# Kernel tuning notes

Measured on AMD Instinct MI355X. Metric: run time of the kernel, lower is better.

The kernel has to match this reference:

```python
import jax, jax.numpy as jnp
import numpy as np

# Paired binary-tree layout over 20 inputs: widths 20->10->5->3->2->1.
# Odd trailing element is carried through unchanged. Node counts per layer
# sum to 19 nodes per tree; 19 trees total.
LAYER_WIDTHS = [20, 10, 5, 3, 2]  # widths at the input of each pairing layer
NODE_COUNTS = [10, 5, 2, 1, 1]    # pairs formed at each layer (sum = 19)
EPS = 1e-6


def setup_inputs() -> dict:
    key = jax.random.key(0)
    k1, k2, k3, k4 = jax.random.split(key, 4)
    B = 1_000_000
    p1 = jax.random.randint(k1, (B,), 0, 10)
    p2 = jax.random.randint(k2, (B,), 0, 10)
    c20 = jax.random.uniform(k3, (B, 20), dtype=jnp.float32)  # fuzzy truth values in [0,1]
    # raw andness params: one per node (19) per tree (19)
    w_raw = jax.random.normal(k4, (19, 19), dtype=jnp.float32)
    return {"p1": p1, "p2": p2, "c20": c20, "w_raw": w_raw}


def _multi_tree_forward(c20, w_raw):
    B = c20.shape[0]
    T = 19  # number of trees
    # andness in (0,1): convex mix between AND (min) and OR (max)
    w = jax.nn.sigmoid(w_raw)  # [T, 19]
    # all 19 trees see the same 20D input -> vectorize trees as a dim
    x = jnp.broadcast_to(c20[:, None, :], (B, T, 20))  # [B, T, 20]
    off = 0
    for width, n in zip(LAYER_WIDTHS, NODE_COUNTS):
        a = x[:, :, 0:2 * n:2]   # left children  [B, T, n]
        b = x[:, :, 1:2 * n:2]   # right children [B, T, n]
        wn = w[:, off:off + n][None, :, :]  # [1, T, n]
        y = wn * jnp.minimum(a, b) + (1.0 - wn) * jnp.maximum(a, b)
        if width % 2 == 1:  # carry the unpaired trailing element through
            y = jnp.concatenate([y, x[:, :, -1:]], axis=-1)
        x = y
        off += n
    out = x[:, :, 0]  # [B, 19] root of each tree
    return jnp.clip(out, EPS, 1.0 - EPS)


def reference(p1, p2, c20, w_raw):
    # p1/p2 are part of the original signature but unused by the forward math
    return _multi_tree_forward(c20, w_raw)
```

## Files before the change

kernel.cpp:

```cpp
#include <hip/hip_runtime.h>

#define EPS_F 1e-6f

__global__ void sigmoid_w_kernel(const float* __restrict__ w_raw,
                                 float* __restrict__ w) {
    int i = threadIdx.x;
    if (i < 361) {
        w[i] = 1.0f / (1.0f + expf(-w_raw[i]));
    }
}

__device__ __forceinline__ float mixf(float a, float b, float wv) {
    float mn = fminf(a, b);
    float mx = fmaxf(a, b);
    return fmaf(wv, mn - mx, mx);
}

__global__ __launch_bounds__(256) void tree_forward_kernel(
    const float* __restrict__ c20,
    const float* __restrict__ w,
    float* __restrict__ out,
    int B)
{
    int s = blockIdx.x * blockDim.x + threadIdx.x;
    if (s >= B) return;

    float x[20];
    const float4* src = reinterpret_cast<const float4*>(c20 + (size_t)s * 20);
    #pragma unroll
    for (int q = 0; q < 5; ++q) {
        float4 v = src[q];
        x[4*q + 0] = v.x;
        x[4*q + 1] = v.y;
        x[4*q + 2] = v.z;
        x[4*q + 3] = v.w;
    }

    float* dst = out + (size_t)s * 19;

    #pragma unroll
    for (int t = 0; t < 19; ++t) {
        const float* wr = w + t * 19;

        float y[10];
        #pragma unroll
        for (int k = 0; k < 10; ++k)
            y[k] = mixf(x[2*k], x[2*k + 1], wr[k]);

        float z[5];
        #pragma unroll
        for (int k = 0; k < 5; ++k)
            z[k] = mixf(y[2*k], y[2*k + 1], wr[10 + k]);

        float u0 = mixf(z[0], z[1], wr[15]);
        float u1 = mixf(z[2], z[3], wr[16]);
        float u2 = z[4];

        float v0 = mixf(u0, u1, wr[17]);

        float r = mixf(v0, u2, wr[18]);

        dst[t] = fminf(fmaxf(r, EPS_F), 1.0f - EPS_F);
    }
}

extern "C" void kernel_launch(void* const* d_in, const int* in_sizes, int n_in,
                              void* d_out, int out_size, void* d_ws, size_t ws_size,
                              hipStream_t stream) {
    const float* c20   = (const float*)d_in[2];
    const float* w_raw = (const float*)d_in[3];
    float* out = (float*)d_out;
    float* w   = (float*)d_ws;

    int B = in_sizes[0];

    sigmoid_w_kernel<<<1, 384, 0, stream>>>(w_raw, w);

    int block = 256;
    int grid = (B + block - 1) / block;
    tree_forward_kernel<<<grid, block, 0, stream>>>(c20, w, out, B);
}
```

Measured before the change: 166.7 us.

## Stage outputs in shared memory for coalesced float4 stores, two samples per thread

```diff
diff --git a/kernel.cpp b/kernel.cpp
--- a/kernel.cpp
+++ b/kernel.cpp
@@ -1,6 +1,8 @@
 #include <hip/hip_runtime.h>
 
 #define EPS_F 1e-6f
+#define BLK   256
+#define SPB   512
 
 __global__ void sigmoid_w_kernel(const float* __restrict__ w_raw,
                                  float* __restrict__ w) {
@@ -16,51 +18,103 @@
     return fmaf(wv, mn - mx, mx);
 }
 
-__global__ __launch_bounds__(256) void tree_forward_kernel(
+__global__ __launch_bounds__(BLK) void tree_forward_kernel(
     const float* __restrict__ c20,
     const float* __restrict__ w,
     float* __restrict__ out,
     int B)
 {
-    int s = blockIdx.x * blockDim.x + threadIdx.x;
-    if (s >= B) return;
+    __shared__ float so[SPB * 19];
 
-    float x[20];
-    const float4* src = reinterpret_cast<const float4*>(c20 + (size_t)s * 20);
-    #pragma unroll
-    for (int q = 0; q < 5; ++q) {
-        float4 v = src[q];
-        x[4*q + 0] = v.x;
-        x[4*q + 1] = v.y;
-        x[4*q + 2] = v.z;
-        x[4*q + 3] = v.w;
+    const int tid = threadIdx.x;
+    const long long S0 = (long long)blockIdx.x * SPB;
+    const long long sA = S0 + tid;
+    const long long sB = S0 + BLK + tid;
+
+    float xa[20], xb[20];
+
+    if (sA < B) {
+        const float4* p = reinterpret_cast<const float4*>(c20 + sA * 20);
+        #pragma unroll
+        for (int q = 0; q < 5; ++q) {
+            float4 v = p[q];
+            xa[4*q+0] = v.x; xa[4*q+1] = v.y; xa[4*q+2] = v.z; xa[4*q+3] = v.w;
+        }
+    } else {
+        #pragma unroll
+        for (int i = 0; i < 20; ++i) xa[i] = 0.0f;
+    }
+    if (sB < B) {
+        const float4* p = reinterpret_cast<const float4*>(c20 + sB * 20);
+        #pragma unroll
+        for (int q = 0; q < 5; ++q) {
+            float4 v = p[q];
+            xb[4*q+0] = v.x; xb[4*q+1] = v.y; xb[4*q+2] = v.z; xb[4*q+3] = v.w;
+        }
+    } else {
+        #pragma unroll
+        for (int i = 0; i < 20; ++i) xb[i] = 0.0f;
     }
 
-    float* dst = out + (size_t)s * 19;
+    float* __restrict__ oA = &so[tid * 19];
+    float* __restrict__ oB = &so[(tid + BLK) * 19];
 
     #pragma unroll
     for (int t = 0; t < 19; ++t) {
         const float* wr = w + t * 19;
 
-        float y[10];
+        float ya[10], yb[10];
         #pragma unroll
-        for (int k = 0; k < 10; ++k)
-            y[k] = mixf(x[2*k], x[2*k + 1], wr[k]);
+        for (int k = 0; k < 10; ++k) {
+            float wv = wr[k];
+            ya[k] = mixf(xa[2*k], xa[2*k+1], wv);
+            yb[k] = mixf(xb[2*k], xb[2*k+1], wv);
+        }
 
-        float z[5];
+        float za[5], zb[5];
         #pragma unroll
-        for (int k = 0; k < 5; ++k)
-            z[k] = mixf(y[2*k], y[2*k + 1], wr[10 + k]);
+        for (int k = 0; k < 5; ++k) {
+            float wv = wr[10 + k];
+            za[k] = mixf(ya[2*k], ya[2*k+1], wv);
+            zb[k] = mixf(yb[2*k], yb[2*k+1], wv);
+        }
 
-        float u0 = mixf(z[0], z[1], wr[15]);
-        float u1 = mixf(z[2], z[3], wr[16]);
-        float u2 = z[4];
+        float w15 = wr[15], w16 = wr[16];
+        float ua0 = mixf(za[0], za[1], w15);
+        float ub0 = mixf(zb[0], zb[1], w15);
+        float ua1 = mixf(za[2], za[3], w16);
+        float ub1 = mixf(zb[2], zb[3], w16);
+        float ua2 = za[4];
+        float ub2 = zb[4];
 
-        float v0 = mixf(u0, u1, wr[17]);
+        float w17 = wr[17];
+        float va = mixf(ua0, ua1, w17);
+        float vb = mixf(ub0, ub1, w17);
 
-        float r = mixf(v0, u2, wr[18]);
+        float w18 = wr[18];
+        float ra = mixf(va, ua2, w18);
+        float rb = mixf(vb, ub2, w18);
 
-        dst[t] = fminf(fmaxf(r, EPS_F), 1.0f - EPS_F);
+        oA[t] = fminf(fmaxf(ra, EPS_F), 1.0f - EPS_F);
+        oB[t] = fminf(fmaxf(rb, EPS_F), 1.0f - EPS_F);
+    }
+
+    __syncthreads();
+
+    const long long nDw    = (long long)B * 19;
+    const long long baseDw = S0 * 19;
+    const float4* ls = reinterpret_cast<const float4*>(so);
+
+    for (int i = tid; i < (SPB * 19) / 4; i += BLK) {
+        long long g = baseDw + (long long)i * 4;
+        if (g + 3 < nDw) {
+            *reinterpret_cast<float4*>(out + g) = ls[i];
+        } else if (g < nDw) {
+            float4 v = ls[i];
+            out[g] = v.x;
+            if (g + 1 < nDw) out[g + 1] = v.y;
+            if (g + 2 < nDw) out[g + 2] = v.z;
+        }
     }
 }
 
@@ -76,7 +130,6 @@
 
     sigmoid_w_kernel<<<1, 384, 0, stream>>>(w_raw, w);
 
-    int block = 256;
-    int grid = (B + block - 1) / block;
-    tree_forward_kernel<<<grid, block, 0, stream>>>(c20, w, out, B);
+    int grid = (B + SPB - 1) / SPB;
+    tree_forward_kernel<<<grid, BLK, 0, stream>>>(c20, w, out, B);
 }
```

New measurement: 158.4 us. 5.0% less time.
